# Kernel optimization log

Measured on AMD Instinct MI355X. Metric: run time of the kernel, lower is better.

The kernel has to match this reference:

```python
import jax, jax.numpy as jnp
import numpy as np

B, N, P, C = 2, 1024, 32, 256   # batch, num queries, in_points, eff_in_dim(=in_dim, G=1)
OP = 32                          # out_points
HID = 128                        # parameter_generator hidden width
TOTAL = C * C + OP * P           # channel + spatial mixing params per query


def setup_inputs() -> dict:
    key = jax.random.key(0)
    ks = jax.random.split(key, 8)
    sc = lambda k, shape, s=0.02: jax.random.normal(k, shape, jnp.float32) * s
    return {
        "x": jax.random.normal(ks[0], (B, N, 1, P, C), jnp.float32),
        "query": jax.random.normal(ks[1], (B, N, C), jnp.float32),
        # LayerNorm initialized unit-norm style (gamma * width**-0.5), bias zero
        "ln_w": jnp.full((C,), C ** -0.5, jnp.float32),
        "ln_b": jnp.zeros((C,), jnp.float32),
        "w1": sc(ks[2], (HID, C)),
        "b1": jnp.zeros((HID,), jnp.float32),
        "w2": sc(ks[3], (TOTAL, HID)),
        "b2": sc(ks[4], (TOTAL,), 0.05),
        "m_beta": jnp.zeros((C,), jnp.float32),
        "s_beta": jnp.zeros((OP,), jnp.float32),
        "proj_w": sc(ks[5], (C, OP * C)),
        "proj_b": jnp.zeros((C,), jnp.float32),
    }


def reference(x, query, ln_w, ln_b, w1, b1, w2, b2, m_beta, s_beta, proj_w, proj_b):
    # parameter_generator: LayerNorm(eps=1e-6) -> Linear(C,128) -> Linear(128,TOTAL)
    mu = jnp.mean(query, axis=-1, keepdims=True)
    var = jnp.var(query, axis=-1, keepdims=True)  # biased, matches torch LayerNorm
    q = (query - mu) * jax.lax.rsqrt(var + 1e-6) * ln_w + ln_b
    h = q @ w1.T + b1                               # [B,N,128]
    params = h @ w2.T + b2                          # [B,N,TOTAL]

    cm = params[..., : C * C].reshape(B, N, C, C)   # channel mixing [B,N,Cin,Cout]
    sm = params[..., C * C :].reshape(B, N, OP, P)  # spatial mixing [B,N,OP,P]

    xs = x[:, :, 0]                                 # [B,N,P,C] (g==1)
    # baddbmm(channel_bias, x, channel_mixing) then GELU (exact erf)
    out = jnp.einsum('bnpc,bncd->bnpd', xs, cm) + m_beta
    out = jax.nn.gelu(out, approximate=False)
    # baddbmm(spatial_bias, spatial_mixing, out) then GELU
    out = jnp.einsum('bnop,bnpd->bnod', sm, out) + s_beta[None, None, :, None]
    out = jax.nn.gelu(out, approximate=False)

    out = out.reshape(B, N, OP * C) @ proj_w.T + proj_b  # tuo_proj -> [B,N,C]
    return out
```

## Files before the change

### kernel.cpp

```cpp
#include <hip/hip_runtime.h>
#include <hip/hip_bf16.h>

#define TKN   2048
#define CDIM  256
#define PDIM  32
#define ODIM  32
#define HIDD  128
#define CCSZ  65536
#define TOTSZ 66560
#define KSPL  16

typedef unsigned short u16;
typedef __bf16 bf16x8 __attribute__((ext_vector_type(8)));
typedef float f32x4 __attribute__((ext_vector_type(4)));
typedef unsigned short u16x4 __attribute__((ext_vector_type(4)));
typedef unsigned short u16x8 __attribute__((ext_vector_type(8)));

__device__ __forceinline__ u16 f2b(float f){
  __hip_bfloat16 h = __float2bfloat16(f);
  return *reinterpret_cast<u16*>(&h);
}
__device__ __forceinline__ float gelu_exact(float x){
  return 0.5f * x * (1.0f + erff(x * 0.70710678118654752f));
}
__device__ __forceinline__ float gelu_fast(float x){
  const float z = 1.5957691216057308f * (x + 0.044715f * x * x * x);
  return x / (1.0f + __expf(-z));
}
__device__ __forceinline__ void gload16(const void* g, void* l){
  __builtin_amdgcn_global_load_lds(
      (const __attribute__((address_space(1))) unsigned int*)g,
      (__attribute__((address_space(3))) unsigned int*)l, 16, 0, 0);
}

__global__ __launch_bounds__(256) void k_prep_h(
    const float* __restrict__ query, const float* __restrict__ ln_w,
    const float* __restrict__ ln_b, const float* __restrict__ w1,
    const float* __restrict__ b1, u16* __restrict__ H){
  const int t = blockIdx.x;
  const int tid = threadIdx.x;
  __shared__ float qs[CDIM];
  __shared__ float red[8];
  __shared__ float stat[2];
  float v = query[(size_t)t*CDIM + tid];
  float s = v, s2 = v*v;
  #pragma unroll
  for(int o=32;o>0;o>>=1){ s += __shfl_down(s,o,64); s2 += __shfl_down(s2,o,64); }
  const int wv = tid>>6;
  if((tid&63)==0){ red[wv]=s; red[4+wv]=s2; }
  __syncthreads();
  if(tid==0){
    float ss=red[0]+red[1]+red[2]+red[3];
    float qq=red[4]+red[5]+red[6]+red[7];
    float mu=ss/(float)CDIM;
    float var=qq/(float)CDIM - mu*mu;
    stat[0]=mu; stat[1]=rsqrtf(var+1e-6f);
  }
  __syncthreads();
  qs[tid] = (v - stat[0])*stat[1]*ln_w[tid] + ln_b[tid];
  __syncthreads();
  if(tid < HIDD){
    const float* wr = w1 + (size_t)tid*CDIM;
    float acc = b1[tid];
    #pragma unroll 8
    for(int c=0;c<CDIM;c++) acc += qs[c]*wr[c];
    H[(size_t)t*HIDD + tid] = f2b(acc);
  }
}

__global__ __launch_bounds__(256) void k_prep_w2(
    const float* __restrict__ w2, const float* __restrict__ b2,
    u16* __restrict__ w2s, float* __restrict__ b2p){
  const int gid = blockIdx.x*256 + threadIdx.x;
  const int n  = gid >> 4;
  const int ch = gid & 15;
  if(n >= TOTSZ) return;
  int j;
  if(n < CCSZ){
    const int f = n >> 9, rem = n & 511;
    const int g = rem >> 7, r = (rem >> 3) & 15, e = rem & 7;
    const int d = (f >> 3)*16 + r;
    const int c = (f & 7)*32 + g*8 + e;
    j = c*256 + d;
  } else {
    j = n;
  }
  const float* src = w2 + (size_t)j*HIDD + ch*8;
  u16x8 tv;
  #pragma unroll
  for(int i=0;i<8;i++) tv[i] = f2b(src[i]);
  const int q = n >> 7, ks = ch >> 2, nt8 = (n >> 4) & 7, kg = ch & 3, r15 = n & 15;
  *(u16x8*)(w2s + ((size_t)((q*4 + ks)*8 + nt8))*512 + (kg*16 + r15)*8) = tv;
  if(ch == 0) b2p[n] = b2[j];
}

__global__ __launch_bounds__(256) void k_prep_pw(
    const float* __restrict__ pw, u16* __restrict__ pwb){
  const int gid = blockIdx.x*256 + threadIdx.x;
  const int e = gid >> 11;
  const int kp = (gid & 2047)*4;
  const int grp = kp >> 8;
  const int rem = kp & 255;
  const int g = rem >> 6, r15 = (rem >> 2) & 15;
  const int w_ = grp >> 2, mt = (grp >> 1) & 1, nt = grp & 1;
  const int o = nt*16 + r15;
  const int d0 = w_*32 + mt*16 + g*4;
  const float* s = pw + (size_t)e*8192 + o*256 + d0;
  u16x4 tv;
  tv[0]=f2b(s[0]); tv[1]=f2b(s[1]); tv[2]=f2b(s[2]); tv[3]=f2b(s[3]);
  *(u16x4*)(pwb + (size_t)e*8192 + kp) = tv;
}

__global__ __launch_bounds__(256, 3) void k_params(
    const u16* __restrict__ H, const u16* __restrict__ w2s,
    const float* __restrict__ b2p, u16* __restrict__ pbuf, int chnk){
  __shared__ __align__(16) u16 S[4][16][136];
  const int tid = threadIdx.x;
  const int lane = tid & 63;
  const int w = tid >> 6;
  const int q = blockIdx.x;
  const int n0 = q * 128;
  const int r15 = lane & 15, g = lane >> 4;
  const int tb = blockIdx.y*128 + w*16;
  bf16x8 afr[2][4];
  #pragma unroll
  for(int m=0;m<2;m++){
    const u16* ap = H + (size_t)(tb + m*64 + r15)*HIDD + g*8;
    #pragma unroll
    for(int ks=0;ks<4;ks++) afr[m][ks] = *(const bf16x8*)(ap + ks*32);
  }
  float b2v[8];
  #pragma unroll
  for(int nt=0;nt<8;nt++) b2v[nt] = b2p[n0 + nt*16 + r15];
  f32x4 acc[2][8] = {};
  #pragma unroll
  for(int ks=0;ks<4;ks++){
    bf16x8 bfr[8];
    #pragma unroll
    for(int nt=0;nt<8;nt++)
      bfr[nt] = *(const bf16x8*)(w2s + ((size_t)((q*4 + ks)*8 + nt))*512 + lane*8);
    #pragma unroll
    for(int m=0;m<2;m++)
      #pragma unroll
      for(int nt=0;nt<8;nt++)
        acc[m][nt] = __builtin_amdgcn_mfma_f32_16x16x32_bf16(afr[m][ks], bfr[nt], acc[m][nt], 0,0,0);
  }
  #pragma unroll
  for(int m=0;m<2;m++){
    #pragma unroll
    for(int nt=0;nt<8;nt++)
      #pragma unroll
      for(int r=0;r<4;r++)
        S[w][g*4 + r][nt*16 + r15] = f2b(acc[m][nt][r] + b2v[nt]);
    u16* dst = pbuf + ((size_t)(q>>2)*chnk + tb + m*64)*512 + (q&3)*128;
    #pragma unroll
    for(int i=0;i<4;i++){
      const int lt = i*4 + (lane >> 4);
      const int jc = lane & 15;
      *(u16x8*)(dst + (size_t)lt*512 + jc*8) = *(const u16x8*)&S[w][lt][jc*8];
    }
  }
}

__global__ __launch_bounds__(512, 2) void k_token(
    const float* __restrict__ xg, const u16* __restrict__ pbuf,
    const float* __restrict__ m_beta, const float* __restrict__ s_beta,
    u16* __restrict__ out2, int chnk){
  __shared__ u16 xs[PDIM][264];
  __shared__ u16 o1[CDIM][36];
  const int tl = blockIdx.x;
  const int tid = threadIdx.x;
  const int lane = tid & 63;
  const int w = tid >> 6;
  const int r15 = lane & 15, g = lane >> 4;

  bf16x8 af[2][8];
  #pragma unroll
  for(int ks=0;ks<8;ks++)
    #pragma unroll
    for(int mt=0;mt<2;mt++){
      const int f = (w*2+mt)*8 + ks;
      af[mt][ks] = *(const bf16x8*)(pbuf + ((size_t)f*chnk + tl)*512 + lane*8);
    }

  {
    const f32x4* src = (const f32x4*)(xg + (size_t)tl*8192);
    #pragma unroll
    for(int i=0;i<4;i++){
      const int idx = tid + 512*i;
      f32x4 v = src[idx];
      const int flat = idx*4;
      const int p = flat >> 8, c = flat & 255;
      u16x4 t4; t4[0]=f2b(v[0]); t4[1]=f2b(v[1]); t4[2]=f2b(v[2]); t4[3]=f2b(v[3]);
      *(u16x4*)&xs[p][c] = t4;
    }
  }
  __syncthreads();

  f32x4 acc[2][2] = {};
  #pragma unroll
  for(int ks=0;ks<8;ks++){
    bf16x8 bf[2];
    #pragma unroll
    for(int nt=0;nt<2;nt++){
      const int p = nt*16 + r15;
      bf[nt] = *(const bf16x8*)&xs[p][ks*32 + g*8];
    }
    #pragma unroll
    for(int mt=0;mt<2;mt++)
      #pragma unroll
      for(int nt=0;nt<2;nt++)
        acc[mt][nt] = __builtin_amdgcn_mfma_f32_16x16x32_bf16(af[mt][ks], bf[nt], acc[mt][nt], 0,0,0);
  }
  bf16x8 bf2[2];
  #pragma unroll
  for(int nt=0;nt<2;nt++){
    const int o = nt*16 + r15;
    const int flat = o*32 + g*8;
    bf2[nt] = *(const bf16x8*)(pbuf + ((size_t)(128 + (flat>>9))*chnk + tl)*512 + (flat & 511));
  }
  #pragma unroll
  for(int mt=0;mt<2;mt++){
    const int d0 = w*32 + mt*16 + g*4;
    const f32x4 mb = *(const f32x4*)&m_beta[d0];
    #pragma unroll
    for(int nt=0;nt<2;nt++){
      const int p = nt*16 + r15;
      #pragma unroll
      for(int r=0;r<4;r++)
        o1[d0+r][p] = f2b(gelu_fast(acc[mt][nt][r] + mb[r]));
    }
  }
  f32x4 acc2[2][2] = {};
  {
    bf16x8 af2[2];
    #pragma unroll
    for(int mt=0;mt<2;mt++){
      const int d = w*32 + mt*16 + r15;
      af2[mt] = *(const bf16x8*)&o1[d][g*8];
    }
    #pragma unroll
    for(int mt=0;mt<2;mt++)
      #pragma unroll
      for(int nt=0;nt<2;nt++)
        acc2[mt][nt] = __builtin_amdgcn_mfma_f32_16x16x32_bf16(af2[mt], bf2[nt], acc2[mt][nt], 0,0,0);
  }
  u16* dst = out2 + (size_t)tl*8192 + w*1024;
  #pragma unroll
  for(int nt=0;nt<2;nt++){
    const float sb = s_beta[nt*16 + r15];
    #pragma unroll
    for(int mt=0;mt<2;mt++){
      u16x4 t4;
      #pragma unroll
      for(int r=0;r<4;r++) t4[r] = f2b(gelu_fast(acc2[mt][nt][r] + sb));
      *(u16x4*)(dst + (mt*2+nt)*256 + lane*4) = t4;
    }
  }
}

__global__ __launch_bounds__(512) void k_proj(
    const u16* __restrict__ out2, const u16* __restrict__ pwb,
    float* __restrict__ part){
  __shared__ u16 Ab[2][64*32];
  __shared__ u16 Bb[2][256*32];
  const int tid = threadIdx.x;
  const int lane = tid & 63, w = tid >> 6;
  const int r15 = lane & 15, g = lane >> 4;
  const int m0 = blockIdx.x * 64;
  const int k0 = blockIdx.y * 512;
  const int wm = (w >> 2) * 32;
  const int wn = (w & 3) * 64;
  const int srow = lane >> 2;
  const int cs   = lane & 3;
  const int a_row = (w & 3)*16 + srow;
  const u16* a_src = out2 + (size_t)(m0 + a_row)*8192 + k0 + (size_t)((cs ^ (a_row & 3))*8);
  const int b_row0 = (2*w)*16 + srow;
  const int b_row1 = (2*w+1)*16 + srow;
  const u16* b_src0 = pwb + (size_t)b_row0*8192 + k0 + (size_t)((cs ^ (b_row0 & 3))*8);
  const u16* b_src1 = pwb + (size_t)b_row1*8192 + k0 + (size_t)((cs ^ (b_row1 & 3))*8);

  f32x4 acc[2][4] = {};

  #define STAGE(buf, kt) do{                                         \
    const int ko = (kt)*32;                                          \
    if(w < 4) gload16(a_src + ko, (char*)&Ab[buf][0] + w*1024);      \
    gload16(b_src0 + ko, (char*)&Bb[buf][0] + (2*w)*1024);           \
    gload16(b_src1 + ko, (char*)&Bb[buf][0] + (2*w+1)*1024);         \
  }while(0)

  STAGE(0, 0);
  __syncthreads();
  int cur = 0;
  for(int kt=0; kt<16; kt++){
    if(kt < 15){ STAGE(cur^1, kt+1); }
    bf16x8 af[2], bf[4];
    #pragma unroll
    for(int mt=0;mt<2;mt++){
      const int row = wm + mt*16 + r15;
      af[mt] = *(const bf16x8*)((char*)&Ab[cur][0] + row*64 + ((g ^ (row&3))*16));
    }
    #pragma unroll
    for(int nt=0;nt<4;nt++){
      const int row = wn + nt*16 + r15;
      bf[nt] = *(const bf16x8*)((char*)&Bb[cur][0] + row*64 + ((g ^ (row&3))*16));
    }
    #pragma unroll
    for(int mt=0;mt<2;mt++)
      #pragma unroll
      for(int nt=0;nt<4;nt++)
        acc[mt][nt] = __builtin_amdgcn_mfma_f32_16x16x32_bf16(af[mt], bf[nt], acc[mt][nt], 0,0,0);
    __syncthreads();
    cur ^= 1;
  }
  #undef STAGE

  float* pbase = part + (size_t)blockIdx.y*TKN*CDIM;
  #pragma unroll
  for(int mt=0;mt<2;mt++)
    #pragma unroll
    for(int nt=0;nt<4;nt++){
      const int t = m0 + wm + mt*16 + g*4;
      const int e = wn + nt*16 + r15;
      #pragma unroll
      for(int r=0;r<4;r++)
        pbase[(size_t)(t+r)*CDIM + e] = acc[mt][nt][r];
    }
}

__global__ __launch_bounds__(256) void k_combine(
    const float* __restrict__ part, const float* __restrict__ pb,
    float* __restrict__ out){
  const int i4 = blockIdx.x*256 + threadIdx.x;
  const int e4 = (i4 & 63)*4;
  f32x4 s = *(const f32x4*)&pb[e4];
  #pragma unroll
  for(int z=0;z<KSPL;z++) s += *(const f32x4*)&part[(size_t)z*524288 + (size_t)i4*4];
  *(f32x4*)&out[(size_t)i4*4] = s;
}

extern "C" void kernel_launch(void* const* d_in, const int* in_sizes, int n_in,
                              void* d_out, int out_size, void* d_ws, size_t ws_size,
                              hipStream_t stream){
  const float* x     = (const float*)d_in[0];
  const float* query = (const float*)d_in[1];
  const float* ln_w  = (const float*)d_in[2];
  const float* ln_b  = (const float*)d_in[3];
  const float* w1    = (const float*)d_in[4];
  const float* b1    = (const float*)d_in[5];
  const float* w2    = (const float*)d_in[6];
  const float* b2    = (const float*)d_in[7];
  const float* m_beta= (const float*)d_in[8];
  const float* s_beta= (const float*)d_in[9];
  const float* pw    = (const float*)d_in[10];
  const float* pb    = (const float*)d_in[11];
  float* out = (float*)d_out;
  char* ws = (char*)d_ws;

  const size_t need_big = 192u*1024u*1024u;
  const int chnk = (ws_size >= need_big) ? 1024 : 256;
  const int nch  = TKN / chnk;

  size_t off = 0;
  u16* H     = (u16*)(ws + off);  off += (size_t)TKN*HIDD*2;
  u16* w2s   = (u16*)(ws + off);  off += (size_t)TOTSZ*HIDD*2;
  float* b2p = (float*)(ws + off);off += (size_t)TOTSZ*4;
  u16* pwb   = (u16*)(ws + off);  off += (size_t)CDIM*8192*2;
  u16* pbuf  = (u16*)(ws + off);  off += (size_t)chnk*TOTSZ*2;
  u16* out2  = (u16*)(ws + off);  off += (size_t)TKN*8192*2;
  float* part= (float*)pbuf;

  k_prep_h<<<TKN, 256, 0, stream>>>(query, ln_w, ln_b, w1, b1, H);
  k_prep_w2<<<4160, 256, 0, stream>>>(w2, b2, w2s, b2p);
  k_prep_pw<<<2048, 256, 0, stream>>>(pw, pwb);
  for(int ch=0; ch<nch; ch++){
    k_params<<<dim3(520, chnk/128), 256, 0, stream>>>(H + (size_t)ch*chnk*HIDD, w2s, b2p, pbuf, chnk);
    k_token<<<chnk, 512, 0, stream>>>(x + (size_t)ch*chnk*8192, pbuf, m_beta, s_beta,
                                      out2 + (size_t)ch*chnk*8192, chnk);
  }
  k_proj<<<dim3(32,KSPL), 512, 0, stream>>>(out2, pwb, part);
  k_combine<<<512, 256, 0, stream>>>(part, pb, out);
}
```

Baseline: 220.1 us.

## Software-pipeline parameter generation and per-token mixing with double-buffered chunks

Merges the parameter-generation GEMM for chunk i and the token-mixing work for chunk i-1 into one launch, with block IDs split between the two roles and the generated parameters double-buffered. This lets the bandwidth-heavy parameter writes overlap the token-mixing compute and removes the serial dependency between the two kernels for each chunk. The chunk size changes from 1024 to 512 under the large-workspace condition, so there are more launches, and the second parameter buffer uses more workspace. Occupancy may also be limited because the fused kernel combines both roles' register and LDS needs.

Measured after the change: 246.9 us. 1.12x slower.

```diff
diff --git a/kernel.cpp b/kernel.cpp
--- a/kernel.cpp
+++ b/kernel.cpp
@@ -19,9 +19,6 @@
 __device__ __forceinline__ u16 f2b(float f){
   __hip_bfloat16 h = __float2bfloat16(f);
   return *reinterpret_cast<u16*>(&h);
-}
-__device__ __forceinline__ float gelu_exact(float x){
-  return 0.5f * x * (1.0f + erff(x * 0.70710678118654752f));
 }
 __device__ __forceinline__ float gelu_fast(float x){
   const float z = 1.5957691216057308f * (x + 0.044715f * x * x * x);
@@ -182,7 +179,6 @@
       const int f = (w*2+mt)*8 + ks;
       af[mt][ks] = *(const bf16x8*)(pbuf + ((size_t)f*chnk + tl)*512 + lane*8);
     }
-
   {
     const f32x4* src = (const f32x4*)(xg + (size_t)tl*8192);
     #pragma unroll
@@ -255,6 +251,153 @@
       #pragma unroll
       for(int r=0;r<4;r++) t4[r] = f2b(gelu_fast(acc2[mt][nt][r] + sb));
       *(u16x4*)(dst + (mt*2+nt)*256 + lane*4) = t4;
+    }
+  }
+}
+
+__global__ __launch_bounds__(512, 2) void k_fused(
+    const float* __restrict__ xg, const u16* __restrict__ pbufR,
+    u16* __restrict__ pbufW, const u16* __restrict__ H,
+    const u16* __restrict__ w2s, const float* __restrict__ b2p,
+    const float* __restrict__ m_beta, const float* __restrict__ s_beta,
+    u16* __restrict__ out2, int chnk, int nP){
+  __shared__ __align__(16) char ldsraw[35328];
+  const int bid = blockIdx.x;
+  const int tid = threadIdx.x;
+  const int lane = tid & 63;
+  const int w = tid >> 6;
+  const int r15 = lane & 15, g = lane >> 4;
+
+  if(bid < nP){
+    u16 (*S)[16][136] = (u16 (*)[16][136])ldsraw;
+    const int nYP = nP / 520;
+    const int q  = bid / nYP;
+    const int y  = bid - q*nYP;
+    const int n0 = q * 128;
+    const int tb = y*256 + w*16;
+    bf16x8 afr[2][4];
+    #pragma unroll
+    for(int m=0;m<2;m++){
+      const u16* ap = H + (size_t)(tb + m*128 + r15)*HIDD + g*8;
+      #pragma unroll
+      for(int ks=0;ks<4;ks++) afr[m][ks] = *(const bf16x8*)(ap + ks*32);
+    }
+    float b2v[8];
+    #pragma unroll
+    for(int nt=0;nt<8;nt++) b2v[nt] = b2p[n0 + nt*16 + r15];
+    f32x4 acc[2][8] = {};
+    #pragma unroll
+    for(int ks=0;ks<4;ks++){
+      bf16x8 bfr[8];
+      #pragma unroll
+      for(int nt=0;nt<8;nt++)
+        bfr[nt] = *(const bf16x8*)(w2s + ((size_t)((q*4 + ks)*8 + nt))*512 + lane*8);
+      #pragma unroll
+      for(int m=0;m<2;m++)
+        #pragma unroll
+        for(int nt=0;nt<8;nt++)
+          acc[m][nt] = __builtin_amdgcn_mfma_f32_16x16x32_bf16(afr[m][ks], bfr[nt], acc[m][nt], 0,0,0);
+    }
+    #pragma unroll
+    for(int m=0;m<2;m++){
+      #pragma unroll
+      for(int nt=0;nt<8;nt++)
+        #pragma unroll
+        for(int r=0;r<4;r++)
+          S[w][g*4 + r][nt*16 + r15] = f2b(acc[m][nt][r] + b2v[nt]);
+      const int t0 = tb + m*128;
+      u16* dst = pbufW + ((size_t)(q>>2)*chnk + t0)*512 + (q&3)*128;
+      #pragma unroll
+      for(int i=0;i<4;i++){
+        const int lt = i*4 + (lane >> 4);
+        const int jc = lane & 15;
+        *(u16x8*)(dst + (size_t)lt*512 + jc*8) = *(const u16x8*)&S[w][lt][jc*8];
+      }
+    }
+  } else {
+    u16 (*xs)[264] = (u16 (*)[264])ldsraw;
+    u16 (*o1)[36]  = (u16 (*)[36])(ldsraw + 16896);
+    const int tl = bid - nP;
+    bf16x8 af[2][8];
+    #pragma unroll
+    for(int ks=0;ks<8;ks++)
+      #pragma unroll
+      for(int mt=0;mt<2;mt++){
+        const int f = (w*2+mt)*8 + ks;
+        af[mt][ks] = *(const bf16x8*)(pbufR + ((size_t)f*chnk + tl)*512 + lane*8);
+      }
+    {
+      const f32x4* src = (const f32x4*)(xg + (size_t)tl*8192);
+      #pragma unroll
+      for(int i=0;i<4;i++){
+        const int idx = tid + 512*i;
+        f32x4 v = src[idx];
+        const int flat = idx*4;
+        const int p = flat >> 8, c = flat & 255;
+        u16x4 t4; t4[0]=f2b(v[0]); t4[1]=f2b(v[1]); t4[2]=f2b(v[2]); t4[3]=f2b(v[3]);
+        *(u16x4*)&xs[p][c] = t4;
+      }
+    }
+    __syncthreads();
+    f32x4 acc[2][2] = {};
+    #pragma unroll
+    for(int ks=0;ks<8;ks++){
+      bf16x8 bf[2];
+      #pragma unroll
+      for(int nt=0;nt<2;nt++){
+        const int p = nt*16 + r15;
+        bf[nt] = *(const bf16x8*)&xs[p][ks*32 + g*8];
+      }
+      #pragma unroll
+      for(int mt=0;mt<2;mt++)
+        #pragma unroll
+        for(int nt=0;nt<2;nt++)
+          acc[mt][nt] = __builtin_amdgcn_mfma_f32_16x16x32_bf16(af[mt][ks], bf[nt], acc[mt][nt], 0,0,0);
+    }
+    bf16x8 bf2[2];
+    #pragma unroll
+    for(int nt=0;nt<2;nt++){
+      const int o = nt*16 + r15;
+      const int flat = o*32 + g*8;
+      bf2[nt] = *(const bf16x8*)(pbufR + ((size_t)(128 + (flat>>9))*chnk + tl)*512 + (flat & 511));
+    }
+    #pragma unroll
+    for(int mt=0;mt<2;mt++){
+      const int d0 = w*32 + mt*16 + g*4;
+      const f32x4 mb = *(const f32x4*)&m_beta[d0];
+      #pragma unroll
+      for(int nt=0;nt<2;nt++){
+        const int p = nt*16 + r15;
+        #pragma unroll
+        for(int r=0;r<4;r++)
+          o1[d0+r][p] = f2b(gelu_fast(acc[mt][nt][r] + mb[r]));
+      }
+    }
+    f32x4 acc2[2][2] = {};
+    {
+      bf16x8 af2[2];
+      #pragma unroll
+      for(int mt=0;mt<2;mt++){
+        const int d = w*32 + mt*16 + r15;
+        af2[mt] = *(const bf16x8*)&o1[d][g*8];
+      }
+      #pragma unroll
+      for(int mt=0;mt<2;mt++)
+        #pragma unroll
+        for(int nt=0;nt<2;nt++)
+          acc2[mt][nt] = __builtin_amdgcn_mfma_f32_16x16x32_bf16(af2[mt], bf2[nt], acc2[mt][nt], 0,0,0);
+    }
+    u16* dst = out2 + (size_t)tl*8192 + w*1024;
+    #pragma unroll
+    for(int nt=0;nt<2;nt++){
+      const float sb = s_beta[nt*16 + r15];
+      #pragma unroll
+      for(int mt=0;mt<2;mt++){
+        u16x4 t4;
+        #pragma unroll
+        for(int r=0;r<4;r++) t4[r] = f2b(gelu_fast(acc2[mt][nt][r] + sb));
+        *(u16x4*)(dst + (mt*2+nt)*256 + lane*4) = t4;
+      }
     }
   }
 }
@@ -357,27 +500,36 @@
   float* out = (float*)d_out;
   char* ws = (char*)d_ws;
 
-  const size_t need_big = 192u*1024u*1024u;
-  const int chnk = (ws_size >= need_big) ? 1024 : 256;
+  const int chnk = (ws_size >= 200u*1024u*1024u) ? 512 : 256;
   const int nch  = TKN / chnk;
+  const int nP   = 520 * (chnk/256);
 
   size_t off = 0;
   u16* H     = (u16*)(ws + off);  off += (size_t)TKN*HIDD*2;
   u16* w2s   = (u16*)(ws + off);  off += (size_t)TOTSZ*HIDD*2;
   float* b2p = (float*)(ws + off);off += (size_t)TOTSZ*4;
   u16* pwb   = (u16*)(ws + off);  off += (size_t)CDIM*8192*2;
-  u16* pbuf  = (u16*)(ws + off);  off += (size_t)chnk*TOTSZ*2;
+  u16* pbuf0 = (u16*)(ws + off);  off += (size_t)chnk*TOTSZ*2;
+  u16* pbuf1 = (u16*)(ws + off);  off += (size_t)chnk*TOTSZ*2;
   u16* out2  = (u16*)(ws + off);  off += (size_t)TKN*8192*2;
-  float* part= (float*)pbuf;
+  float* part= (float*)pbuf0;
+  u16* pbufs[2] = {pbuf0, pbuf1};
 
   k_prep_h<<<TKN, 256, 0, stream>>>(query, ln_w, ln_b, w1, b1, H);
   k_prep_w2<<<4160, 256, 0, stream>>>(w2, b2, w2s, b2p);
   k_prep_pw<<<2048, 256, 0, stream>>>(pw, pwb);
-  for(int ch=0; ch<nch; ch++){
-    k_params<<<dim3(520, chnk/128), 256, 0, stream>>>(H + (size_t)ch*chnk*HIDD, w2s, b2p, pbuf, chnk);
-    k_token<<<chnk, 512, 0, stream>>>(x + (size_t)ch*chnk*8192, pbuf, m_beta, s_beta,
-                                      out2 + (size_t)ch*chnk*8192, chnk);
-  }
+
+  k_params<<<dim3(520, chnk/128), 256, 0, stream>>>(H, w2s, b2p, pbufs[0], chnk);
+  for(int i=1; i<nch; i++){
+    k_fused<<<nP + chnk, 512, 0, stream>>>(
+        x + (size_t)(i-1)*chnk*8192, pbufs[(i-1)&1], pbufs[i&1],
+        H + (size_t)i*chnk*HIDD, w2s, b2p, m_beta, s_beta,
+        out2 + (size_t)(i-1)*chnk*8192, chnk, nP);
+  }
+  k_token<<<chnk, 512, 0, stream>>>(x + (size_t)(nch-1)*chnk*8192, pbufs[(nch-1)&1],
+                                    m_beta, s_beta,
+                                    out2 + (size_t)(nch-1)*chnk*8192, chnk);
+
   k_proj<<<dim3(32,KSPL), 512, 0, stream>>>(out2, pwb, part);
   k_combine<<<512, 256, 0, stream>>>(part, pb, out);
 }
```
